# Performance work log

Measured on AMD Instinct MI355X. Metric: run time of the kernel, lower is better.

Reference implementation:

```python
import jax, jax.numpy as jnp
import numpy as np

NC_MEM = 64          # nTemporalMemoryChannels
NC_IMG = 64          # nImageFeatureChannels
FTL_RATIO = 0.5      # temporalFTLRatio
N_BLOCKS = 3         # nTemporalBlocks
B, H, W = 32, 64, 96
M = 32               # memory buffer length (= max(memory_idx)+1)


def setup_inputs() -> dict:
    key = jax.random.key(0)
    ks = jax.random.split(key, 8)
    eye = jnp.eye(4, dtype=jnp.float32)
    img_features = jax.random.normal(ks[0], (B, NC_IMG, H, W), jnp.float32)
    prev_mem_features = jax.random.normal(ks[1], (M, NC_MEM, H, W), jnp.float32)
    # extrinsics: random perturbation around identity so torch.inverse-equivalent is well conditioned
    prev_extrinsics = 0.1 * jax.random.normal(ks[2], (M, 4, 4), jnp.float32) + eye
    cur_extrinsics = 0.1 * jax.random.normal(ks[3], (B, 4, 4), jnp.float32) + eye
    memory_idx = jnp.arange(B, dtype=jnp.int32)
    use_memory = jax.random.randint(ks[4], (B,), 0, 2).astype(bool)
    NC = NC_MEM + NC_IMG
    Ws = jax.random.normal(ks[5], (N_BLOCKS, NC, NC), jnp.float32) * (1.0 / np.sqrt(NC))
    bs = jax.random.normal(ks[6], (N_BLOCKS, NC), jnp.float32) * 0.01
    return {
        "img_features": img_features,
        "prev_mem_features": prev_mem_features,
        "prev_extrinsics": prev_extrinsics,
        "cur_extrinsics": cur_extrinsics,
        "memory_idx": memory_idx,
        "use_memory": use_memory,
        "Ws": Ws,
        "bs": bs,
    }


def _apply_ftl(xf, feats, ratio):
    # Feature Transform Layer: first `ratio` fraction of channels (rounded down
    # to a multiple of 4) treated as groups of homogeneous 4-vectors per pixel,
    # warped by the 4x4 transform xf; remaining channels pass through.
    b, c, h, w = feats.shape
    nc_ftl = (int(c * ratio) // 4) * 4
    g = nc_ftl // 4
    pts = feats[:, :nc_ftl].reshape(b, g, 4, h * w)
    pts = jnp.einsum("bij,bgjp->bgip", xf, pts).reshape(b, nc_ftl, h, w)
    return jnp.concatenate([pts, feats[:, nc_ftl:]], axis=1)


def reference(img_features, prev_mem_features, prev_extrinsics, cur_extrinsics,
              memory_idx, use_memory, Ws, bs):
    eye = jnp.eye(4, dtype=prev_extrinsics.dtype)
    # --- transform_memory_features (gather + extrinsics warp, masked) ---
    mem_g = prev_mem_features[memory_idx]              # [B, NC_MEM, H, W]
    prev_ext_g = prev_extrinsics[memory_idx]           # [B, 4, 4]
    # entries with use_memory=False are zeroed; guard inverse with identity
    safe_prev = jnp.where(use_memory[:, None, None], prev_ext_g, eye)
    prev_cam0_to_world = jnp.linalg.inv(safe_prev)
    xf = jnp.einsum("bij,bjk->bik", cur_extrinsics, prev_cam0_to_world)
    mem_xfed = _apply_ftl(xf, mem_g, FTL_RATIO)
    mem_xfed = jnp.where(use_memory[:, None, None, None], mem_xfed,
                         jnp.zeros((), mem_xfed.dtype))
    # --- forward_one_step: concat + 1x1 conv stack (pointwise matmuls) ---
    x = jnp.concatenate([mem_xfed, img_features], axis=1)  # [B, 128, H, W]
    n = Ws.shape[0]
    for i in range(n):
        x = jnp.einsum("oc,bchw->bohw", Ws[i], x) + bs[i][None, :, None, None]
        if i != n - 1:
            x = jax.nn.relu(x)
    fused_features = x[:, NC_MEM:]                     # returned output
    return fused_features
```

## Files before the change

### kernel.cpp

```cpp
#include <hip/hip_runtime.h>
#include <hip/hip_fp16.h>

#define NC_MEM 64
#define NC_IMG 64
#define NC     128
#define B_     32
#define H_     64
#define W_     96
#define HW_    (H_ * W_)
#define P_TILE 128
#define NTILES (HW_ / P_TILE)
#define FS     520
#define FOFF(pt, ks) ((((pt) * 4) + (ks)) * FS)
#define XOFF(pt, ks, blk) (FOFF(pt, ks) + ((((blk) + (pt)) & 63) << 3))

#define WA_HI  0
#define WA_LO  98304
#define XF_OFF 196608
#define UM_OFF 198656

typedef _Float16 f16x8 __attribute__((ext_vector_type(8)));
typedef __attribute__((ext_vector_type(4))) float f32x4;

__device__ inline unsigned pk2h(float a, float b) {
    __half2 h = __floats2half2_rn(a, b);
    return *(const unsigned*)&h;
}

__device__ inline void bar_lds() {
    __builtin_amdgcn_sched_barrier(0);
    asm volatile("s_waitcnt lgkmcnt(0)" ::: "memory");
    __builtin_amdgcn_s_barrier();
    asm volatile("" ::: "memory");
    __builtin_amdgcn_sched_barrier(0);
}

__global__ void prep(const float* __restrict__ Ws,
                     const float* __restrict__ prev_ext,
                     const float* __restrict__ cur_ext,
                     const int* __restrict__ mem_idx,
                     const unsigned char* __restrict__ um_raw,
                     unsigned char* __restrict__ wsb) {
    if (blockIdx.x < 192) {
        int idx = blockIdx.x * 256 + threadIdx.x;
        int l = idx >> 14, r = idx & 16383, o = r >> 7, c = r & 127;
        float w = Ws[idx];
        __half hi = __float2half_rn(w);
        __half lo = __float2half_rn(w - __half2float(hi));
        int mt = o >> 4, lm = o & 15, ks = c >> 5, kr = c & 31, q = kr >> 3, j = kr & 7;
        int lane = q * 16 + lm;
        int di = ((((l * 8 + mt) * 4 + ks) * 64 + lane) << 3) + j;
        ((unsigned short*)(wsb + WA_HI))[di] = __half_as_ushort(hi);
        ((unsigned short*)(wsb + WA_LO))[di] = __half_as_ushort(lo);
        return;
    }
    int tb = threadIdx.x;
    if (tb >= 64) return;
    bool flag = (tb < 32) && (tb & 3) && (um_raw[tb] != 0);
    bool is_bool = __any(flag);
    if (tb >= B_) return;
    int b = tb;
    bool um = is_bool ? (um_raw[b] != 0) : (((const int*)um_raw)[b] != 0);
    int mi = mem_idx[b];

    float a[16];
#pragma unroll
    for (int i = 0; i < 16; ++i)
        a[i] = um ? prev_ext[mi * 16 + i] : ((i % 5 == 0) ? 1.f : 0.f);

    float s0 = a[0]*a[5]  - a[1]*a[4];
    float s1 = a[0]*a[6]  - a[2]*a[4];
    float s2 = a[0]*a[7]  - a[3]*a[4];
    float s3 = a[1]*a[6]  - a[2]*a[5];
    float s4 = a[1]*a[7]  - a[3]*a[5];
    float s5 = a[2]*a[7]  - a[3]*a[6];
    float c5 = a[10]*a[15] - a[11]*a[14];
    float c4 = a[9]*a[15]  - a[11]*a[13];
    float c3 = a[9]*a[14]  - a[10]*a[13];
    float c2 = a[8]*a[15]  - a[11]*a[12];
    float c1 = a[8]*a[14]  - a[10]*a[12];
    float c0 = a[8]*a[13]  - a[9]*a[12];
    float det = s0*c5 - s1*c4 + s2*c3 + s3*c2 - s4*c1 + s5*c0;
    float id = 1.0f / det;

    float inv[16];
    inv[0]  = ( a[5]*c5  - a[6]*c4  + a[7]*c3)  * id;
    inv[1]  = (-a[1]*c5  + a[2]*c4  - a[3]*c3)  * id;
    inv[2]  = ( a[13]*s5 - a[14]*s4 + a[15]*s3) * id;
    inv[3]  = (-a[9]*s5  + a[10]*s4 - a[11]*s3) * id;
    inv[4]  = (-a[4]*c5  + a[6]*c2  - a[7]*c1)  * id;
    inv[5]  = ( a[0]*c5  - a[2]*c2  + a[3]*c1)  * id;
    inv[6]  = (-a[12]*s5 + a[14]*s2 - a[15]*s1) * id;
    inv[7]  = ( a[8]*s5  - a[10]*s2 + a[11]*s1) * id;
    inv[8]  = ( a[4]*c4  - a[5]*c2  + a[7]*c0)  * id;
    inv[9]  = (-a[0]*c4  + a[1]*c2  - a[3]*c0)  * id;
    inv[10] = ( a[12]*s4 - a[13]*s2 + a[15]*s0) * id;
    inv[11] = (-a[8]*s4  + a[9]*s2  - a[11]*s0) * id;
    inv[12] = (-a[4]*c3  + a[5]*c1  - a[6]*c0)  * id;
    inv[13] = ( a[0]*c3  - a[1]*c1  + a[2]*c0)  * id;
    inv[14] = (-a[12]*s3 + a[13]*s1 - a[14]*s0) * id;
    inv[15] = ( a[8]*s3  - a[9]*s1  + a[10]*s0) * id;

    float* xf = (float*)(wsb + XF_OFF) + b * 16;
#pragma unroll
    for (int i = 0; i < 4; ++i)
#pragma unroll
        for (int j2 = 0; j2 < 4; ++j2) {
            float s = 0.f;
#pragma unroll
            for (int k = 0; k < 4; ++k)
                s += cur_ext[b * 16 + i * 4 + k] * inv[k * 4 + j2];
            xf[i * 4 + j2] = s;
        }
    ((float*)(wsb + UM_OFF))[b] = um ? 1.f : 0.f;
}

__global__ __launch_bounds__(512, 4)
void fused_main(const float* __restrict__ img, const float* __restrict__ mem,
                const int* __restrict__ mem_idx, const float* __restrict__ bs,
                const unsigned char* __restrict__ wsb, float* __restrict__ out) {
    __shared__ unsigned short xh[32 * FS];

    const int t   = threadIdx.x;
    const int b   = blockIdx.y;
    const int hw0 = blockIdx.x * P_TILE;
    const bool umb = ((const float*)(wsb + UM_OFF))[b] != 0.f;
    const int mi  = mem_idx[b];

    const f16x8* __restrict__ WH = (const f16x8*)(wsb + WA_HI);
    const f16x8* __restrict__ WL = (const f16x8*)(wsb + WA_LO);

    const int w    = t >> 6;
    const int lane = t & 63;
    const int wq   = lane >> 4;
    const int lm   = lane & 15;
    const int mt0  = 2 * (w & 3);
    const int nt0  = 4 * (w >> 2);

#define FI(l, mt, ks) (((((l) * 8 + (mt)) * 4) + (ks)) * 64 + lane)

    {
        const int q   = ((t & 7) << 2) | ((t >> 3) & 3);
        const int og  = t >> 5;
        const int px0 = hw0 + q * 4;
        const int pt  = q >> 2;
        if (umb) {
            const int c0 = og * 8;
            const float* basep = (c0 < NC_MEM)
                ? (mem + ((size_t)mi * NC_MEM + c0) * HW_ + px0)
                : (img + ((size_t)b * NC_IMG + (c0 - NC_MEM)) * HW_ + px0);
            f32x4 v[8];
#pragma unroll
            for (int cc = 0; cc < 8; ++cc)
                v[cc] = *(const f32x4*)(basep + (size_t)cc * HW_);
            if (og < 4) {
                float xfv[16];
                const float* xfp = (const float*)(wsb + XF_OFF) + b * 16;
#pragma unroll
                for (int j = 0; j < 4; ++j)
                    *(f32x4*)&xfv[j * 4] = *(const f32x4*)&xfp[j * 4];
#pragma unroll
                for (int sg = 0; sg < 2; ++sg) {
#pragma unroll
                    for (int i = 0; i < 4; ++i) {
                        float a0 = v[4*sg+0][i], a1 = v[4*sg+1][i];
                        float a2 = v[4*sg+2][i], a3 = v[4*sg+3][i];
                        v[4*sg+0][i] = xfv[0]*a0  + xfv[1]*a1  + xfv[2]*a2  + xfv[3]*a3;
                        v[4*sg+1][i] = xfv[4]*a0  + xfv[5]*a1  + xfv[6]*a2  + xfv[7]*a3;
                        v[4*sg+2][i] = xfv[8]*a0  + xfv[9]*a1  + xfv[10]*a2 + xfv[11]*a3;
                        v[4*sg+3][i] = xfv[12]*a0 + xfv[13]*a1 + xfv[14]*a2 + xfv[15]*a3;
                    }
                }
            }
            const int bk0 = (og & 3) * 16 + (q & 3) * 4;
#pragma unroll
            for (int i = 0; i < 4; ++i) {
                uint4 pk;
                pk.x = pk2h(v[0][i], v[1][i]);
                pk.y = pk2h(v[2][i], v[3][i]);
                pk.z = pk2h(v[4][i], v[5][i]);
                pk.w = pk2h(v[6][i], v[7][i]);
                *(uint4*)&xh[XOFF(pt, og >> 2, bk0 + i)] = pk;
            }
        } else {
            const int gg = 16 + og;
            const int c0 = gg * 4 - NC_MEM;
            f32x4 u[4];
#pragma unroll
            for (int cc = 0; cc < 4; ++cc)
                u[cc] = *(const f32x4*)(img + ((size_t)b * NC_IMG + c0 + cc) * HW_ + px0);
            const int bk0 = ((gg & 7) >> 1) * 16 + (q & 3) * 4;
            const int hoff = (gg & 1) * 4;
#pragma unroll
            for (int i = 0; i < 4; ++i)
                *(uint2*)&xh[XOFF(pt, gg >> 3, bk0 + i) + hoff] =
                    make_uint2(pk2h(u[0][i], u[1][i]), pk2h(u[2][i], u[3][i]));
        }
    }

    const unsigned short* bp[4];
#pragma unroll
    for (int nt = 0; nt < 4; ++nt)
        bp[nt] = &xh[XOFF(nt0 + nt, 0, lane)];

    const int kpa = umb ? 0 : 2, kpb = umb ? 1 : 3;
    f16x8 p0h = WH[FI(0, mt0,     kpa)], p0l = WL[FI(0, mt0,     kpa)];
    f16x8 p1h = WH[FI(0, mt0 + 1, kpa)], p1l = WL[FI(0, mt0 + 1, kpa)];
    f16x8 p2h = WH[FI(0, mt0,     kpb)], p2l = WL[FI(0, mt0,     kpb)];
    f16x8 p3h = WH[FI(0, mt0 + 1, kpb)], p3l = WL[FI(0, mt0 + 1, kpb)];

    bar_lds();

    f32x4 acc[2][4];

    auto run_ks = [&](int ks, f16x8 ah0, f16x8 al0, f16x8 ah1, f16x8 al1) {
#pragma unroll
        for (int nt = 0; nt < 4; ++nt) {
            f16x8 bh = *(const f16x8*)(bp[nt] + ks * FS);
            acc[0][nt] = __builtin_amdgcn_mfma_f32_16x16x32_f16(ah0, bh, acc[0][nt], 0, 0, 0);
            acc[1][nt] = __builtin_amdgcn_mfma_f32_16x16x32_f16(ah1, bh, acc[1][nt], 0, 0, 0);
            acc[0][nt] = __builtin_amdgcn_mfma_f32_16x16x32_f16(al0, bh, acc[0][nt], 0, 0, 0);
            acc[1][nt] = __builtin_amdgcn_mfma_f32_16x16x32_f16(al1, bh, acc[1][nt], 0, 0, 0);
        }
    };
    auto writeback = [&]() {
#pragma unroll
        for (int mi2 = 0; mi2 < 2; ++mi2) {
            const int mt = mt0 + mi2;
            const int ks2 = mt >> 1;
            const int lane_f = ((mt & 1) * 2 + (wq >> 1)) * 16 + lm;
            const int j0 = (wq & 1) * 4;
#pragma unroll
            for (int nt = 0; nt < 4; ++nt) {
                float v0 = fmaxf(acc[mi2][nt][0], 0.f);
                float v1 = fmaxf(acc[mi2][nt][1], 0.f);
                float v2 = fmaxf(acc[mi2][nt][2], 0.f);
                float v3 = fmaxf(acc[mi2][nt][3], 0.f);
                *(uint2*)&xh[XOFF(nt0 + nt, ks2, lane_f) + j0] =
                    make_uint2(pk2h(v0, v1), pk2h(v2, v3));
            }
        }
    };

#pragma unroll
    for (int mi2 = 0; mi2 < 2; ++mi2) {
        f32x4 bv = *(const f32x4*)&bs[0 * NC + (mt0 + mi2) * 16 + wq * 4];
#pragma unroll
        for (int nt = 0; nt < 4; ++nt) acc[mi2][nt] = bv;
    }
    __builtin_amdgcn_s_setprio(1);
    if (umb) {
        run_ks(0, p0h, p0l, p1h, p1l);
        run_ks(1, p2h, p2l, p3h, p3l);
        run_ks(2, WH[FI(0, mt0, 2)], WL[FI(0, mt0, 2)],
                  WH[FI(0, mt0 + 1, 2)], WL[FI(0, mt0 + 1, 2)]);
        run_ks(3, WH[FI(0, mt0, 3)], WL[FI(0, mt0, 3)],
                  WH[FI(0, mt0 + 1, 3)], WL[FI(0, mt0 + 1, 3)]);
    } else {
        run_ks(2, p0h, p0l, p1h, p1l);
        run_ks(3, p2h, p2l, p3h, p3l);
    }
    __builtin_amdgcn_s_setprio(0);
    f16x8 q0h = WH[FI(1, mt0, 0)],     q0l = WL[FI(1, mt0, 0)];
    f16x8 q1h = WH[FI(1, mt0 + 1, 0)], q1l = WL[FI(1, mt0 + 1, 0)];
    f16x8 q2h = WH[FI(1, mt0, 1)],     q2l = WL[FI(1, mt0, 1)];
    f16x8 q3h = WH[FI(1, mt0 + 1, 1)], q3l = WL[FI(1, mt0 + 1, 1)];
    bar_lds();
    writeback();
    bar_lds();

#pragma unroll
    for (int mi2 = 0; mi2 < 2; ++mi2) {
        f32x4 bv = *(const f32x4*)&bs[1 * NC + (mt0 + mi2) * 16 + wq * 4];
#pragma unroll
        for (int nt = 0; nt < 4; ++nt) acc[mi2][nt] = bv;
    }
    __builtin_amdgcn_s_setprio(1);
    run_ks(0, q0h, q0l, q1h, q1l);
    run_ks(1, q2h, q2l, q3h, q3l);
    run_ks(2, WH[FI(1, mt0, 2)], WL[FI(1, mt0, 2)],
              WH[FI(1, mt0 + 1, 2)], WL[FI(1, mt0 + 1, 2)]);
    run_ks(3, WH[FI(1, mt0, 3)], WL[FI(1, mt0, 3)],
              WH[FI(1, mt0 + 1, 3)], WL[FI(1, mt0 + 1, 3)]);
    __builtin_amdgcn_s_setprio(0);
    const int mt2 = 4 + (w & 3);
    f16x8 r0h = WH[FI(2, mt2, 0)], r0l = WL[FI(2, mt2, 0)];
    f16x8 r1h = WH[FI(2, mt2, 1)], r1l = WL[FI(2, mt2, 1)];
    f16x8 r2h = WH[FI(2, mt2, 2)], r2l = WL[FI(2, mt2, 2)];
    f16x8 r3h = WH[FI(2, mt2, 3)], r3l = WL[FI(2, mt2, 3)];
    bar_lds();
    writeback();
    bar_lds();

    {
        f32x4 a2[4];
        f32x4 bv = *(const f32x4*)&bs[2 * NC + mt2 * 16 + wq * 4];
#pragma unroll
        for (int nt = 0; nt < 4; ++nt) a2[nt] = bv;
        auto run2 = [&](int ks, f16x8 ah, f16x8 al) {
#pragma unroll
            for (int nt = 0; nt < 4; ++nt) {
                f16x8 bh = *(const f16x8*)(bp[nt] + ks * FS);
                a2[nt] = __builtin_amdgcn_mfma_f32_16x16x32_f16(ah, bh, a2[nt], 0, 0, 0);
                a2[nt] = __builtin_amdgcn_mfma_f32_16x16x32_f16(al, bh, a2[nt], 0, 0, 0);
            }
        };
        __builtin_amdgcn_s_setprio(1);
        run2(0, r0h, r0l);
        run2(1, r1h, r1l);
        run2(2, r2h, r2l);
        run2(3, r3h, r3l);
        __builtin_amdgcn_s_setprio(0);
        const int oc0 = mt2 * 16 + wq * 4 - 64;
#pragma unroll
        for (int nt = 0; nt < 4; ++nt) {
            float* dst = out + ((size_t)b * 64 + oc0) * HW_ + hw0 + (nt0 + nt) * 16 + lm;
#pragma unroll
            for (int r = 0; r < 4; ++r)
                __builtin_nontemporal_store(a2[nt][r], dst + (size_t)r * HW_);
        }
    }
#undef FI
}

extern "C" void kernel_launch(void* const* d_in, const int* in_sizes, int n_in,
                              void* d_out, int out_size, void* d_ws, size_t ws_size,
                              hipStream_t stream) {
    const float* img  = (const float*)d_in[0];
    const float* mem  = (const float*)d_in[1];
    const float* pext = (const float*)d_in[2];
    const float* cext = (const float*)d_in[3];
    const int*   midx = (const int*)d_in[4];
    const unsigned char* umem = (const unsigned char*)d_in[5];
    const float* Ws   = (const float*)d_in[6];
    const float* bs   = (const float*)d_in[7];
    float* out = (float*)d_out;
    unsigned char* wsb = (unsigned char*)d_ws;

    hipLaunchKernelGGL(prep, dim3(193), dim3(256), 0, stream,
                       Ws, pext, cext, midx, umem, wsb);
    hipLaunchKernelGGL(fused_main, dim3(NTILES, B_), dim3(512), 0, stream,
                       img, mem, midx, bs, wsb, out);
}
```

Measured before the change: 163.8 us.

## Warp-specialize producer/consumer waves with double-buffered LDS over three pixel tiles

Each block now processes three 128-pixel tiles instead of one. Waves 0-3 run all three MFMA layers over all 8 pixel sub-tiles, while waves 4-7 load and convert the next tile's input into a second LDS buffer. Barrier counts are matched between the two groups. The goal is to hide global-load latency behind compute and to amortise the weight loads across tiles. In exchange, half the waves now do the matrix work, each compute wave holds twice as many accumulators, LDS use doubles, and the grid has a third as many blocks.

After: 227.0 us. 1.39x slower.

```diff
diff --git a/kernel.cpp b/kernel.cpp
--- a/kernel.cpp
+++ b/kernel.cpp
@@ -9,7 +9,7 @@
 #define W_     96
 #define HW_    (H_ * W_)
 #define P_TILE 128
-#define NTILES (HW_ / P_TILE)
+#define T_BLK  3
 #define FS     520
 #define FOFF(pt, ks) ((((pt) * 4) + (ks)) * FS)
 #define XOFF(pt, ks, blk) (FOFF(pt, ks) + ((((blk) + (pt)) & 63) << 3))
@@ -119,46 +119,51 @@
 void fused_main(const float* __restrict__ img, const float* __restrict__ mem,
                 const int* __restrict__ mem_idx, const float* __restrict__ bs,
                 const unsigned char* __restrict__ wsb, float* __restrict__ out) {
-    __shared__ unsigned short xh[32 * FS];
-
-    const int t   = threadIdx.x;
-    const int b   = blockIdx.y;
-    const int hw0 = blockIdx.x * P_TILE;
+    __shared__ unsigned short xh[2][32 * FS];
+
+    const int t    = threadIdx.x;
+    const int b    = blockIdx.y;
+    const int hw00 = blockIdx.x * (P_TILE * T_BLK);
     const bool umb = ((const float*)(wsb + UM_OFF))[b] != 0.f;
-    const int mi  = mem_idx[b];
+    const int mi   = mem_idx[b];
 
     const f16x8* __restrict__ WH = (const f16x8*)(wsb + WA_HI);
     const f16x8* __restrict__ WL = (const f16x8*)(wsb + WA_LO);
 
-    const int w    = t >> 6;
     const int lane = t & 63;
     const int wq   = lane >> 4;
     const int lm   = lane & 15;
-    const int mt0  = 2 * (w & 3);
-    const int nt0  = 4 * (w >> 2);
+
+    const int cw   = (t >> 6) & 3;
+    const int mt0  = 2 * cw;
+    const int mt2  = 4 + cw;
+    const int tp   = t & 255;
+    const int q    = tp & 31;
+    const int og2  = tp >> 5;
+    const int pt   = q >> 2;
 
 #define FI(l, mt, ks) (((((l) * 8 + (mt)) * 4) + (ks)) * 64 + lane)
 
-    {
-        const int q   = ((t & 7) << 2) | ((t >> 3) & 3);
-        const int og  = t >> 5;
-        const int px0 = hw0 + q * 4;
-        const int pt  = q >> 2;
+    auto stage_load = [&](int hw0t, int og, f32x4* v) {
+        const int px0 = hw0t + q * 4;
         if (umb) {
             const int c0 = og * 8;
             const float* basep = (c0 < NC_MEM)
                 ? (mem + ((size_t)mi * NC_MEM + c0) * HW_ + px0)
                 : (img + ((size_t)b * NC_IMG + (c0 - NC_MEM)) * HW_ + px0);
-            f32x4 v[8];
 #pragma unroll
             for (int cc = 0; cc < 8; ++cc)
                 v[cc] = *(const f32x4*)(basep + (size_t)cc * HW_);
+        } else {
+            const int c0 = og * 4;
+#pragma unroll
+            for (int cc = 0; cc < 4; ++cc)
+                v[cc] = *(const f32x4*)(img + ((size_t)b * NC_IMG + c0 + cc) * HW_ + px0);
+        }
+    };
+    auto stage_write = [&](unsigned short* xb, int og, f32x4* v, const float* xfv) {
+        if (umb) {
             if (og < 4) {
-                float xfv[16];
-                const float* xfp = (const float*)(wsb + XF_OFF) + b * 16;
-#pragma unroll
-                for (int j = 0; j < 4; ++j)
-                    *(f32x4*)&xfv[j * 4] = *(const f32x4*)&xfp[j * 4];
 #pragma unroll
                 for (int sg = 0; sg < 2; ++sg) {
 #pragma unroll
@@ -180,144 +185,172 @@
                 pk.y = pk2h(v[2][i], v[3][i]);
                 pk.z = pk2h(v[4][i], v[5][i]);
                 pk.w = pk2h(v[6][i], v[7][i]);
-                *(uint4*)&xh[XOFF(pt, og >> 2, bk0 + i)] = pk;
+                *(uint4*)&xb[XOFF(pt, og >> 2, bk0 + i)] = pk;
             }
         } else {
             const int gg = 16 + og;
-            const int c0 = gg * 4 - NC_MEM;
-            f32x4 u[4];
-#pragma unroll
-            for (int cc = 0; cc < 4; ++cc)
-                u[cc] = *(const f32x4*)(img + ((size_t)b * NC_IMG + c0 + cc) * HW_ + px0);
             const int bk0 = ((gg & 7) >> 1) * 16 + (q & 3) * 4;
             const int hoff = (gg & 1) * 4;
 #pragma unroll
             for (int i = 0; i < 4; ++i)
-                *(uint2*)&xh[XOFF(pt, gg >> 3, bk0 + i) + hoff] =
-                    make_uint2(pk2h(u[0][i], u[1][i]), pk2h(u[2][i], u[3][i]));
-        }
-    }
-
-    const unsigned short* bp[4];
-#pragma unroll
-    for (int nt = 0; nt < 4; ++nt)
-        bp[nt] = &xh[XOFF(nt0 + nt, 0, lane)];
-
-    const int kpa = umb ? 0 : 2, kpb = umb ? 1 : 3;
-    f16x8 p0h = WH[FI(0, mt0,     kpa)], p0l = WL[FI(0, mt0,     kpa)];
-    f16x8 p1h = WH[FI(0, mt0 + 1, kpa)], p1l = WL[FI(0, mt0 + 1, kpa)];
-    f16x8 p2h = WH[FI(0, mt0,     kpb)], p2l = WL[FI(0, mt0,     kpb)];
-    f16x8 p3h = WH[FI(0, mt0 + 1, kpb)], p3l = WL[FI(0, mt0 + 1, kpb)];
-
-    bar_lds();
-
-    f32x4 acc[2][4];
-
-    auto run_ks = [&](int ks, f16x8 ah0, f16x8 al0, f16x8 ah1, f16x8 al1) {
-#pragma unroll
-        for (int nt = 0; nt < 4; ++nt) {
-            f16x8 bh = *(const f16x8*)(bp[nt] + ks * FS);
-            acc[0][nt] = __builtin_amdgcn_mfma_f32_16x16x32_f16(ah0, bh, acc[0][nt], 0, 0, 0);
-            acc[1][nt] = __builtin_amdgcn_mfma_f32_16x16x32_f16(ah1, bh, acc[1][nt], 0, 0, 0);
-            acc[0][nt] = __builtin_amdgcn_mfma_f32_16x16x32_f16(al0, bh, acc[0][nt], 0, 0, 0);
-            acc[1][nt] = __builtin_amdgcn_mfma_f32_16x16x32_f16(al1, bh, acc[1][nt], 0, 0, 0);
+                *(uint2*)&xb[XOFF(pt, gg >> 3, bk0 + i) + hoff] =
+                    make_uint2(pk2h(v[0][i], v[1][i]), pk2h(v[2][i], v[3][i]));
         }
     };
-    auto writeback = [&]() {
-#pragma unroll
-        for (int mi2 = 0; mi2 < 2; ++mi2) {
-            const int mt = mt0 + mi2;
-            const int ks2 = mt >> 1;
-            const int lane_f = ((mt & 1) * 2 + (wq >> 1)) * 16 + lm;
-            const int j0 = (wq & 1) * 4;
-#pragma unroll
-            for (int nt = 0; nt < 4; ++nt) {
-                float v0 = fmaxf(acc[mi2][nt][0], 0.f);
-                float v1 = fmaxf(acc[mi2][nt][1], 0.f);
-                float v2 = fmaxf(acc[mi2][nt][2], 0.f);
-                float v3 = fmaxf(acc[mi2][nt][3], 0.f);
-                *(uint2*)&xh[XOFF(nt0 + nt, ks2, lane_f) + j0] =
-                    make_uint2(pk2h(v0, v1), pk2h(v2, v3));
-            }
-        }
-    };
-
-#pragma unroll
-    for (int mi2 = 0; mi2 < 2; ++mi2) {
-        f32x4 bv = *(const f32x4*)&bs[0 * NC + (mt0 + mi2) * 16 + wq * 4];
-#pragma unroll
-        for (int nt = 0; nt < 4; ++nt) acc[mi2][nt] = bv;
-    }
-    __builtin_amdgcn_s_setprio(1);
-    if (umb) {
-        run_ks(0, p0h, p0l, p1h, p1l);
-        run_ks(1, p2h, p2l, p3h, p3l);
-        run_ks(2, WH[FI(0, mt0, 2)], WL[FI(0, mt0, 2)],
-                  WH[FI(0, mt0 + 1, 2)], WL[FI(0, mt0 + 1, 2)]);
-        run_ks(3, WH[FI(0, mt0, 3)], WL[FI(0, mt0, 3)],
-                  WH[FI(0, mt0 + 1, 3)], WL[FI(0, mt0 + 1, 3)]);
+
+    if (t < 256) {
+        int bo[8];
+#pragma unroll
+        for (int nt = 0; nt < 8; ++nt)
+            bo[nt] = XOFF(nt, 0, lane);
+
+        const int kpa = umb ? 0 : 2, kpb = umb ? 1 : 3;
+        f16x8 p0h = WH[FI(0, mt0,     kpa)], p0l = WL[FI(0, mt0,     kpa)];
+        f16x8 p1h = WH[FI(0, mt0 + 1, kpa)], p1l = WL[FI(0, mt0 + 1, kpa)];
+        f16x8 p2h = WH[FI(0, mt0,     kpb)], p2l = WL[FI(0, mt0,     kpb)];
+        f16x8 p3h = WH[FI(0, mt0 + 1, kpb)], p3l = WL[FI(0, mt0 + 1, kpb)];
+
+        bar_lds();
+
+        f32x4 acc[2][8];
+        auto runk8 = [&](const unsigned short* xc, int ks,
+                         f16x8 ah0, f16x8 al0, f16x8 ah1, f16x8 al1) {
+#pragma unroll
+            for (int nt = 0; nt < 8; ++nt) {
+                f16x8 bh = *(const f16x8*)&xc[bo[nt] + ks * FS];
+                acc[0][nt] = __builtin_amdgcn_mfma_f32_16x16x32_f16(ah0, bh, acc[0][nt], 0, 0, 0);
+                acc[1][nt] = __builtin_amdgcn_mfma_f32_16x16x32_f16(ah1, bh, acc[1][nt], 0, 0, 0);
+                acc[0][nt] = __builtin_amdgcn_mfma_f32_16x16x32_f16(al0, bh, acc[0][nt], 0, 0, 0);
+                acc[1][nt] = __builtin_amdgcn_mfma_f32_16x16x32_f16(al1, bh, acc[1][nt], 0, 0, 0);
+            }
+        };
+        auto writeback = [&](unsigned short* xb) {
+#pragma unroll
+            for (int mi2 = 0; mi2 < 2; ++mi2) {
+                const int mt = mt0 + mi2;
+                const int ks2 = mt >> 1;
+                const int lane_f = ((mt & 1) * 2 + (wq >> 1)) * 16 + lm;
+                const int j0 = (wq & 1) * 4;
+#pragma unroll
+                for (int nt = 0; nt < 8; ++nt) {
+                    float v0 = fmaxf(acc[mi2][nt][0], 0.f);
+                    float v1 = fmaxf(acc[mi2][nt][1], 0.f);
+                    float v2 = fmaxf(acc[mi2][nt][2], 0.f);
+                    float v3 = fmaxf(acc[mi2][nt][3], 0.f);
+                    *(uint2*)&xb[XOFF(nt, ks2, lane_f) + j0] =
+                        make_uint2(pk2h(v0, v1), pk2h(v2, v3));
+                }
+            }
+        };
+
+#pragma unroll
+        for (int tt = 0; tt < T_BLK; ++tt) {
+            unsigned short* xc = xh[tt & 1];
+            const int hw0t = hw00 + tt * P_TILE;
+
+#pragma unroll
+            for (int mi2 = 0; mi2 < 2; ++mi2) {
+                f32x4 bv = *(const f32x4*)&bs[0 * NC + (mt0 + mi2) * 16 + wq * 4];
+#pragma unroll
+                for (int nt = 0; nt < 8; ++nt) acc[mi2][nt] = bv;
+            }
+            __builtin_amdgcn_s_setprio(1);
+            if (umb) {
+                runk8(xc, 0, p0h, p0l, p1h, p1l);
+                runk8(xc, 1, p2h, p2l, p3h, p3l);
+                runk8(xc, 2, WH[FI(0, mt0, 2)], WL[FI(0, mt0, 2)],
+                             WH[FI(0, mt0 + 1, 2)], WL[FI(0, mt0 + 1, 2)]);
+                runk8(xc, 3, WH[FI(0, mt0, 3)], WL[FI(0, mt0, 3)],
+                             WH[FI(0, mt0 + 1, 3)], WL[FI(0, mt0 + 1, 3)]);
+            } else {
+                runk8(xc, 2, p0h, p0l, p1h, p1l);
+                runk8(xc, 3, p2h, p2l, p3h, p3l);
+            }
+            __builtin_amdgcn_s_setprio(0);
+            bar_lds();
+            writeback(xc);
+            bar_lds();
+#pragma unroll
+            for (int mi2 = 0; mi2 < 2; ++mi2) {
+                f32x4 bv = *(const f32x4*)&bs[1 * NC + (mt0 + mi2) * 16 + wq * 4];
+#pragma unroll
+                for (int nt = 0; nt < 8; ++nt) acc[mi2][nt] = bv;
+            }
+            __builtin_amdgcn_s_setprio(1);
+            runk8(xc, 0, WH[FI(1, mt0, 0)], WL[FI(1, mt0, 0)],
+                         WH[FI(1, mt0 + 1, 0)], WL[FI(1, mt0 + 1, 0)]);
+            runk8(xc, 1, WH[FI(1, mt0, 1)], WL[FI(1, mt0, 1)],
+                         WH[FI(1, mt0 + 1, 1)], WL[FI(1, mt0 + 1, 1)]);
+            runk8(xc, 2, WH[FI(1, mt0, 2)], WL[FI(1, mt0, 2)],
+                         WH[FI(1, mt0 + 1, 2)], WL[FI(1, mt0 + 1, 2)]);
+            runk8(xc, 3, WH[FI(1, mt0, 3)], WL[FI(1, mt0, 3)],
+                         WH[FI(1, mt0 + 1, 3)], WL[FI(1, mt0 + 1, 3)]);
+            __builtin_amdgcn_s_setprio(0);
+            bar_lds();
+            writeback(xc);
+            bar_lds();
+            {
+                f32x4 a2[8];
+                f32x4 bv = *(const f32x4*)&bs[2 * NC + mt2 * 16 + wq * 4];
+#pragma unroll
+                for (int nt = 0; nt < 8; ++nt) a2[nt] = bv;
+                __builtin_amdgcn_s_setprio(1);
+#pragma unroll
+                for (int ks = 0; ks < 4; ++ks) {
+                    f16x8 ah = WH[FI(2, mt2, ks)], al = WL[FI(2, mt2, ks)];
+#pragma unroll
+                    for (int nt = 0; nt < 8; ++nt) {
+                        f16x8 bh = *(const f16x8*)&xc[bo[nt] + ks * FS];
+                        a2[nt] = __builtin_amdgcn_mfma_f32_16x16x32_f16(ah, bh, a2[nt], 0, 0, 0);
+                        a2[nt] = __builtin_amdgcn_mfma_f32_16x16x32_f16(al, bh, a2[nt], 0, 0, 0);
+                    }
+                }
+                __builtin_amdgcn_s_setprio(0);
+                const int oc0 = mt2 * 16 + wq * 4 - 64;
+#pragma unroll
+                for (int nt = 0; nt < 8; ++nt) {
+                    float* dst = out + ((size_t)b * 64 + oc0) * HW_ + hw0t + nt * 16 + lm;
+#pragma unroll
+                    for (int r = 0; r < 4; ++r)
+                        __builtin_nontemporal_store(a2[nt][r], dst + (size_t)r * HW_);
+                }
+            }
+            bar_lds();
+        }
     } else {
-        run_ks(2, p0h, p0l, p1h, p1l);
-        run_ks(3, p2h, p2l, p3h, p3l);
-    }
-    __builtin_amdgcn_s_setprio(0);
-    f16x8 q0h = WH[FI(1, mt0, 0)],     q0l = WL[FI(1, mt0, 0)];
-    f16x8 q1h = WH[FI(1, mt0 + 1, 0)], q1l = WL[FI(1, mt0 + 1, 0)];
-    f16x8 q2h = WH[FI(1, mt0, 1)],     q2l = WL[FI(1, mt0, 1)];
-    f16x8 q3h = WH[FI(1, mt0 + 1, 1)], q3l = WL[FI(1, mt0 + 1, 1)];
-    bar_lds();
-    writeback();
-    bar_lds();
-
-#pragma unroll
-    for (int mi2 = 0; mi2 < 2; ++mi2) {
-        f32x4 bv = *(const f32x4*)&bs[1 * NC + (mt0 + mi2) * 16 + wq * 4];
-#pragma unroll
-        for (int nt = 0; nt < 4; ++nt) acc[mi2][nt] = bv;
-    }
-    __builtin_amdgcn_s_setprio(1);
-    run_ks(0, q0h, q0l, q1h, q1l);
-    run_ks(1, q2h, q2l, q3h, q3l);
-    run_ks(2, WH[FI(1, mt0, 2)], WL[FI(1, mt0, 2)],
-              WH[FI(1, mt0 + 1, 2)], WL[FI(1, mt0 + 1, 2)]);
-    run_ks(3, WH[FI(1, mt0, 3)], WL[FI(1, mt0, 3)],
-              WH[FI(1, mt0 + 1, 3)], WL[FI(1, mt0 + 1, 3)]);
-    __builtin_amdgcn_s_setprio(0);
-    const int mt2 = 4 + (w & 3);
-    f16x8 r0h = WH[FI(2, mt2, 0)], r0l = WL[FI(2, mt2, 0)];
-    f16x8 r1h = WH[FI(2, mt2, 1)], r1l = WL[FI(2, mt2, 1)];
-    f16x8 r2h = WH[FI(2, mt2, 2)], r2l = WL[FI(2, mt2, 2)];
-    f16x8 r3h = WH[FI(2, mt2, 3)], r3l = WL[FI(2, mt2, 3)];
-    bar_lds();
-    writeback();
-    bar_lds();
-
-    {
-        f32x4 a2[4];
-        f32x4 bv = *(const f32x4*)&bs[2 * NC + mt2 * 16 + wq * 4];
-#pragma unroll
-        for (int nt = 0; nt < 4; ++nt) a2[nt] = bv;
-        auto run2 = [&](int ks, f16x8 ah, f16x8 al) {
-#pragma unroll
-            for (int nt = 0; nt < 4; ++nt) {
-                f16x8 bh = *(const f16x8*)(bp[nt] + ks * FS);
-                a2[nt] = __builtin_amdgcn_mfma_f32_16x16x32_f16(ah, bh, a2[nt], 0, 0, 0);
-                a2[nt] = __builtin_amdgcn_mfma_f32_16x16x32_f16(al, bh, a2[nt], 0, 0, 0);
-            }
-        };
-        __builtin_amdgcn_s_setprio(1);
-        run2(0, r0h, r0l);
-        run2(1, r1h, r1l);
-        run2(2, r2h, r2l);
-        run2(3, r3h, r3l);
-        __builtin_amdgcn_s_setprio(0);
-        const int oc0 = mt2 * 16 + wq * 4 - 64;
-#pragma unroll
-        for (int nt = 0; nt < 4; ++nt) {
-            float* dst = out + ((size_t)b * 64 + oc0) * HW_ + hw0 + (nt0 + nt) * 16 + lm;
-#pragma unroll
-            for (int r = 0; r < 4; ++r)
-                __builtin_nontemporal_store(a2[nt][r], dst + (size_t)r * HW_);
+        float xfv[16];
+        if (umb) {
+            const float* xfp = (const float*)(wsb + XF_OFF) + b * 16;
+#pragma unroll
+            for (int j = 0; j < 4; ++j)
+                *(f32x4*)&xfv[j * 4] = *(const f32x4*)&xfp[j * 4];
+        }
+        {
+            f32x4 v[8];
+            stage_load(hw00, og2, v);
+            stage_write(xh[0], og2, v, xfv);
+            stage_load(hw00, og2 + 8, v);
+            stage_write(xh[0], og2 + 8, v, xfv);
+        }
+        bar_lds();
+
+#pragma unroll
+        for (int tt = 0; tt < T_BLK; ++tt) {
+            unsigned short* xn = xh[(tt + 1) & 1];
+            f32x4 v0[8], v1[8];
+            bar_lds();
+            if (tt + 1 < T_BLK) {
+                stage_load(hw00 + (tt + 1) * P_TILE, og2,     v0);
+                stage_load(hw00 + (tt + 1) * P_TILE, og2 + 8, v1);
+            }
+            bar_lds();
+            bar_lds();
+            if (tt + 1 < T_BLK) {
+                stage_write(xn, og2,     v0, xfv);
+                stage_write(xn, og2 + 8, v1, xfv);
+            }
+            bar_lds();
+            bar_lds();
         }
     }
 #undef FI
@@ -339,6 +372,6 @@
 
     hipLaunchKernelGGL(prep, dim3(193), dim3(256), 0, stream,
                        Ws, pext, cext, midx, umem, wsb);
-    hipLaunchKernelGGL(fused_main, dim3(NTILES, B_), dim3(512), 0, stream,
+    hipLaunchKernelGGL(fused_main, dim3(HW_ / (P_TILE * T_BLK), B_), dim3(512), 0, stream,
                        img, mem, midx, bs, wsb, out);
 }
```
